# Performance work log

Hardware: AMD Instinct MI355X
Metric: run time of the kernel (lower is better)

## Reference

```python
import jax, jax.numpy as jnp
import numpy as np

EMBED_DIM = 1024
NUM_HEADS = 16
HEAD_DIM = EMBED_DIM // NUM_HEADS
B, T = 2, 2048


def setup_inputs() -> dict:
    key = jax.random.key(0)
    kx, kqkv, kout = jax.random.split(key, 3)
    x = jax.random.normal(kx, (B, T, EMBED_DIM), dtype=jnp.float32)
    # torch Linear(in, out, bias=False): y = x @ W.T, W ~ U(-1/sqrt(in), 1/sqrt(in)).
    # Store pre-transposed as (in, out) for direct matmul.
    bound = 1.0 / np.sqrt(EMBED_DIM)
    w_qkv = jax.random.uniform(kqkv, (EMBED_DIM, 3 * EMBED_DIM), dtype=jnp.float32, minval=-bound, maxval=bound)
    w_out = jax.random.uniform(kout, (EMBED_DIM, EMBED_DIM), dtype=jnp.float32, minval=-bound, maxval=bound)
    return {"x": x, "w_qkv": w_qkv, "w_out": w_out}


def reference(x, w_qkv, w_out):
    Bx, Tx, C = x.shape
    qkv = x @ w_qkv  # (B, T, 3C)
    q, k, v = jnp.split(qkv, 3, axis=-1)

    def split_heads(t):
        return t.reshape(Bx, Tx, NUM_HEADS, HEAD_DIM).transpose(0, 2, 1, 3)  # (B,H,T,hd)

    q, k, v = split_heads(q), split_heads(k), split_heads(v)
    scale = 1.0 / jnp.sqrt(jnp.float32(HEAD_DIM))
    scores = jnp.einsum("bhqd,bhkd->bhqk", q, k) * scale  # (B,H,T,T)
    causal = jnp.tril(jnp.ones((Tx, Tx), dtype=bool))  # True = keep
    scores = jnp.where(causal, scores, jnp.float32(-jnp.inf))
    weights = jax.nn.softmax(scores, axis=-1)
    out = jnp.einsum("bhqk,bhkd->bhqd", weights, v)  # (B,H,T,hd)
    out = out.transpose(0, 2, 1, 3).reshape(Bx, Tx, C)
    return out @ w_out
```

## Files before the change

kernel.cpp:

```cpp
#include <hip/hip_runtime.h>
#include <hip/hip_bf16.h>
#include <stdint.h>
#include <math.h>

#define B_ 2
#define T_ 2048
#define C_ 1024
#define H_ 16
#define HD_ 64
#define BT_ (B_*T_)
#define N1_ (3*C_)

typedef unsigned short u16;
typedef uint32_t u32;
typedef __attribute__((ext_vector_type(8))) short bf16x8;
typedef __attribute__((ext_vector_type(4))) float f32x4;
typedef __attribute__((ext_vector_type(16))) float f32x16;
typedef __attribute__((ext_vector_type(4))) unsigned int u32x4;

__device__ __forceinline__ u16 f2bf(float f) {
  __hip_bfloat16 h = __float2bfloat16(f);
  return *reinterpret_cast<u16*>(&h);
}
__device__ __forceinline__ float bf2f(u16 u) {
  u32 w = ((u32)u) << 16;
  return *reinterpret_cast<float*>(&w);
}
__device__ __forceinline__ u32 cvtpk(float lo, float hi) {
  u32 r;
  asm("v_cvt_pk_bf16_f32 %0, %1, %2" : "=v"(r) : "v"(lo), "v"(hi));
  return r;
}
__device__ __forceinline__ float exp2v(float x) {
  float r;
  asm("v_exp_f32 %0, %1" : "=v"(r) : "v"(x));
  return r;
}

__device__ __forceinline__ void gload_lds16(const void* g, void* l) {
  __builtin_amdgcn_global_load_lds(
      (const __attribute__((address_space(1))) uint32_t*)g,
      (__attribute__((address_space(3))) uint32_t*)l, 16, 0, 0);
}

#define BARX() do { asm volatile("" ::: "memory"); __builtin_amdgcn_s_barrier(); \
                    asm volatile("" ::: "memory"); } while (0)
#define LGKM0() do { asm volatile("s_waitcnt lgkmcnt(0)" ::: "memory"); \
                     __builtin_amdgcn_sched_barrier(0); } while (0)

__global__ __launch_bounds__(256) void prep_k(const float* __restrict__ x,
                                              const float* __restrict__ w_qkv,
                                              const float* __restrict__ w_out,
                                              u16* __restrict__ xb,
                                              u16* __restrict__ wqkvT,
                                              u16* __restrict__ woutT) {
  __shared__ float tile[32][33];
  int bid = blockIdx.x;
  if (bid < 4096) {
    int idx = bid * 1024 + threadIdx.x * 4;
    float4 v = *reinterpret_cast<const float4*>(x + idx);
    u16 tmp[4] = {f2bf(v.x), f2bf(v.y), f2bf(v.z), f2bf(v.w)};
    *reinterpret_cast<uint2*>(xb + idx) = *reinterpret_cast<const uint2*>(tmp);
    return;
  }
  const float* w;
  u16* wt;
  int N, tb;
  if (bid < 7168) { tb = bid - 4096; w = w_qkv; wt = wqkvT; N = N1_; }
  else            { tb = bid - 7168; w = w_out; wt = woutT; N = C_;  }
  int nx = N >> 5;
  int n0 = (tb % nx) * 32, k0 = (tb / nx) * 32;
  int tx = threadIdx.x & 31, ty = threadIdx.x >> 5;
#pragma unroll
  for (int i = 0; i < 4; i++)
    tile[ty + i*8][tx] = w[(size_t)(k0 + ty + i*8) * N + n0 + tx];
  __syncthreads();
#pragma unroll
  for (int i = 0; i < 4; i++)
    wt[(size_t)(n0 + ty + i*8) * 1024 + k0 + tx] = f2bf(tile[tx][ty + i*8]);
}

__global__ __launch_bounds__(512, 2) void gemm256(const u16* __restrict__ A, const u16* __restrict__ Bt,
                                                  u16* __restrict__ Cc) {
  __shared__ u16 As[2][256*64];
  __shared__ u16 Bs[2][192*64];
  int tid = threadIdx.x, w = tid >> 6, lane = tid & 63;
  int m0 = blockIdx.y * 256, n0 = blockIdx.x * 192;
  int wm = (w >> 2) * 128, wn = (w & 3) * 48;
  f32x4 acc[8][3] = {};

  size_t aoff[4];
  size_t boff[3];
#pragma unroll
  for (int i = 0; i < 4; i++) {
    int c = i*512 + tid, row = c >> 3;
    aoff[i] = (size_t)(m0 + row) * 1024 + (size_t)((((c & 7) ^ (row & 7))) * 8);
  }
#pragma unroll
  for (int i = 0; i < 3; i++) {
    int c = i*512 + tid, row = c >> 3;
    boff[i] = (size_t)(n0 + row) * 1024 + (size_t)((((c & 7) ^ (row & 7))) * 8);
  }
  int dstc = w * 1024;

  int r15 = lane & 15, kq = lane >> 4;
  int slot0 = (kq ^ (r15 & 7)) * 8;
  int abase = (wm + r15) * 64;
  int bbase = (wn + r15) * 64;

#pragma unroll
  for (int i = 0; i < 4; i++)
    gload_lds16(A + aoff[i], (char*)&As[0][0] + i*8192 + dstc);
#pragma unroll
  for (int i = 0; i < 3; i++)
    gload_lds16(Bt + boff[i], (char*)&Bs[0][0] + i*8192 + dstc);

  for (int t = 0; t < 16; ++t) {
    int buf = t & 1;
    const u16* Ab = &As[buf][0];
    const u16* Bb = &Bs[buf][0];
    int slot1 = slot0 ^ 32;
    bf16x8 af[8], bfv[3];

    asm volatile("s_waitcnt vmcnt(0)" ::: "memory");
    BARX();

#pragma unroll
    for (int nf = 0; nf < 3; nf++) bfv[nf] = *reinterpret_cast<const bf16x8*>(&Bb[bbase + nf*1024 + slot0]);
#pragma unroll
    for (int mf = 0; mf < 8; mf++) af[mf] = *reinterpret_cast<const bf16x8*>(&Ab[abase + mf*1024 + slot0]);
    if (t < 15) {
      int ko = (t + 1) * 64;
#pragma unroll
      for (int i = 0; i < 4; i++)
        gload_lds16(A + aoff[i] + ko, (char*)&As[buf ^ 1][0] + i*8192 + dstc);
#pragma unroll
      for (int i = 0; i < 3; i++)
        gload_lds16(Bt + boff[i] + ko, (char*)&Bs[buf ^ 1][0] + i*8192 + dstc);
    }
    BARX();
    LGKM0();
    __builtin_amdgcn_s_setprio(1);
#pragma unroll
    for (int mf = 0; mf < 8; mf++)
#pragma unroll
      for (int nf = 0; nf < 3; nf++)
        acc[mf][nf] = __builtin_amdgcn_mfma_f32_16x16x32_bf16(af[mf], bfv[nf], acc[mf][nf], 0, 0, 0);
    __builtin_amdgcn_s_setprio(0);

#pragma unroll
    for (int nf = 0; nf < 3; nf++) bfv[nf] = *reinterpret_cast<const bf16x8*>(&Bb[bbase + nf*1024 + slot1]);
#pragma unroll
    for (int mf = 0; mf < 8; mf++) af[mf] = *reinterpret_cast<const bf16x8*>(&Ab[abase + mf*1024 + slot1]);
    BARX();
    LGKM0();
    __builtin_amdgcn_s_setprio(1);
#pragma unroll
    for (int mf = 0; mf < 8; mf++)
#pragma unroll
      for (int nf = 0; nf < 3; nf++)
        acc[mf][nf] = __builtin_amdgcn_mfma_f32_16x16x32_bf16(af[mf], bfv[nf], acc[mf][nf], 0, 0, 0);
    __builtin_amdgcn_s_setprio(0);
  }

  int rg = kq * 4;
#pragma unroll
  for (int mf = 0; mf < 8; mf++)
#pragma unroll
    for (int nf = 0; nf < 3; nf++) {
      size_t basei = (size_t)(m0 + wm + mf*16 + rg) * N1_ + (size_t)(n0 + wn + nf*16 + r15);
#pragma unroll
      for (int r = 0; r < 4; r++)
        Cc[basei + (size_t)r * N1_] = f2bf(acc[mf][nf][r]);
    }
}

__global__ __launch_bounds__(512, 1) void gemm128(const u16* __restrict__ A, const u16* __restrict__ Bt,
                                                  float* __restrict__ Co) {
  __shared__ u16 As[2][128*64];
  __shared__ u16 Bs[2][128*64];
  int tid = threadIdx.x, w = tid >> 6, lane = tid & 63;
  int m0 = blockIdx.y * 128, n0 = blockIdx.x * 128;
  int wm = (w >> 2) * 64, wn = (w & 3) * 32;
  f32x4 acc[4][2] = {};

  size_t aoff[2], boff[2];
#pragma unroll
  for (int i = 0; i < 2; i++) {
    int c = i*512 + tid, row = c >> 3;
    aoff[i] = (size_t)(m0 + row) * 1024 + (size_t)((((c & 7) ^ (row & 7))) * 8);
    boff[i] = (size_t)(n0 + row) * 1024 + (size_t)((((c & 7) ^ (row & 7))) * 8);
  }
  int dstc = w * 1024;

  int r15 = lane & 15, kq = lane >> 4;
  int slot0 = (kq ^ (r15 & 7)) * 8;
  int abase = (wm + r15) * 64;
  int bbase = (wn + r15) * 64;

#pragma unroll
  for (int i = 0; i < 2; i++) {
    gload_lds16(A  + aoff[i], (char*)&As[0][0] + i*8192 + dstc);
    gload_lds16(Bt + boff[i], (char*)&Bs[0][0] + i*8192 + dstc);
  }

  for (int t = 0; t < 16; ++t) {
    int buf = t & 1;
    const u16* Ab = &As[buf][0];
    const u16* Bb = &Bs[buf][0];
    int slot1 = slot0 ^ 32;
    bf16x8 af[4], bfv[2];

    asm volatile("s_waitcnt vmcnt(0)" ::: "memory");
    BARX();

#pragma unroll
    for (int nf = 0; nf < 2; nf++) bfv[nf] = *reinterpret_cast<const bf16x8*>(&Bb[bbase + nf*1024 + slot0]);
#pragma unroll
    for (int mf = 0; mf < 4; mf++) af[mf] = *reinterpret_cast<const bf16x8*>(&Ab[abase + mf*1024 + slot0]);
    if (t < 15) {
      int ko = (t + 1) * 64;
#pragma unroll
      for (int i = 0; i < 2; i++) {
        gload_lds16(A  + aoff[i] + ko, (char*)&As[buf ^ 1][0] + i*8192 + dstc);
        gload_lds16(Bt + boff[i] + ko, (char*)&Bs[buf ^ 1][0] + i*8192 + dstc);
      }
    }
    BARX();
    LGKM0();
    __builtin_amdgcn_s_setprio(1);
#pragma unroll
    for (int mf = 0; mf < 4; mf++)
#pragma unroll
      for (int nf = 0; nf < 2; nf++)
        acc[mf][nf] = __builtin_amdgcn_mfma_f32_16x16x32_bf16(af[mf], bfv[nf], acc[mf][nf], 0, 0, 0);
    __builtin_amdgcn_s_setprio(0);

#pragma unroll
    for (int nf = 0; nf < 2; nf++) bfv[nf] = *reinterpret_cast<const bf16x8*>(&Bb[bbase + nf*1024 + slot1]);
#pragma unroll
    for (int mf = 0; mf < 4; mf++) af[mf] = *reinterpret_cast<const bf16x8*>(&Ab[abase + mf*1024 + slot1]);
    BARX();
    LGKM0();
    __builtin_amdgcn_s_setprio(1);
#pragma unroll
    for (int mf = 0; mf < 4; mf++)
#pragma unroll
      for (int nf = 0; nf < 2; nf++)
        acc[mf][nf] = __builtin_amdgcn_mfma_f32_16x16x32_bf16(af[mf], bfv[nf], acc[mf][nf], 0, 0, 0);
    __builtin_amdgcn_s_setprio(0);
  }

  int rg = kq * 4;
#pragma unroll
  for (int mf = 0; mf < 4; mf++)
#pragma unroll
    for (int nf = 0; nf < 2; nf++) {
      size_t basei = (size_t)(m0 + wm + mf*16 + rg) * C_ + (size_t)(n0 + wn + nf*16 + r15);
#pragma unroll
      for (int r = 0; r < 4; r++)
        Co[basei + (size_t)r * C_] = acc[mf][nf][r];
    }
}

__global__ __launch_bounds__(256, 2) void attn_kernel(const u16* __restrict__ qkv, u16* __restrict__ attnout) {
  __shared__ u16 Sm[4][4096];
  int tid = threadIdx.x;
  int w = tid >> 6, lane = tid & 63;
  int q31 = lane & 31, hi = lane >> 5;
  int lid = blockIdx.x;
  int xcd = lid & 7, j = lid >> 3;
  int bh = xcd * 4 + (j & 3);
  int p = j >> 2;
  int b = bh >> 4, h = bh & 15;
  const u16* base = qkv + (size_t)b * T_ * N1_;

  u16* Ks = Sm[w];
  u32* Vt32 = reinterpret_cast<u32*>(Sm[w] + 2048);

  const u16* ksrc = base + C_ + h*HD_ + (size_t)(lane >> 3) * N1_
                    + (size_t)(((lane & 7) ^ ((lane >> 3) & 7)) * 8);
  int kp2 = lane & 15, dc = (lane >> 4) * 16;
  int vcs = kp2 >> 2, vkl = kp2 & 3;
  int vflip = (lane >> 4) & 1;
  const u16* vsrc = base + 2*C_ + h*HD_ + (size_t)(2*kp2) * N1_ + dc;
  const float QSC = 0.125f * 1.44269504088896f;
  int swr = (q31 >> 1) & 3;
  int q31f = q31 ^ ((q31 >> 4) & 1);

  int sA = 63 - p, sB = p;
  int qgA = sA * 32 + q31, qgB = sB * 32 + q31;
  int nktU = sA + 1;

  bf16x8 qfA[4], qfB[4];
  {
    const u16* qrowA = base + (size_t)qgA * N1_ + h * HD_;
    const u16* qrowB = base + (size_t)qgB * N1_ + h * HD_;
#pragma unroll
    for (int kk = 0; kk < 4; kk++) {
      bf16x8 ra = *reinterpret_cast<const bf16x8*>(qrowA + kk*16 + hi*8);
      bf16x8 rb = *reinterpret_cast<const bf16x8*>(qrowB + kk*16 + hi*8);
      const u16* pa = (const u16*)&ra;
      const u16* pb = (const u16*)&rb;
      u32x4 qa, qb;
#pragma unroll
      for (int jj = 0; jj < 4; jj++) {
        qa[jj] = cvtpk(bf2f(pa[2*jj]) * QSC, bf2f(pa[2*jj+1]) * QSC);
        qb[jj] = cvtpk(bf2f(pb[2*jj]) * QSC, bf2f(pb[2*jj+1]) * QSC);
      }
      qfA[kk] = __builtin_bit_cast(bf16x8, qa);
      qfB[kk] = __builtin_bit_cast(bf16x8, qb);
    }
  }

  f32x16 oaccA[2] = {}, oaccB[2] = {};
  float lA = 0.f, lB = 0.f;

  bf16x8 vA[2], vB[2];
  {
    size_t off0 = (size_t)(w * 32) * N1_;
#pragma unroll
    for (int r = 0; r < 4; r++)
      gload_lds16(ksrc + off0 + (size_t)(8*r) * N1_, (char*)Ks + r*1024);
#pragma unroll
    for (int r = 0; r < 2; r++) {
      vA[r] = *reinterpret_cast<const bf16x8*>(vsrc + off0 + r*8);
      vB[r] = *reinterpret_cast<const bf16x8*>(vsrc + off0 + r*8 + N1_);
    }
  }

  for (int kt = w; kt < nktU; kt += 4) {
    int kb = kt * 32;
    bool lastown = (kt + 4 >= nktU);
    bool actB = (kt <= sB);

    asm volatile("s_waitcnt vmcnt(4)" ::: "memory");

    f32x16 stA = {}, stB = {};
    if (actB) {
#pragma unroll
      for (int kk = 0; kk < 4; kk++) {
        bf16x8 kf = *reinterpret_cast<const bf16x8*>(
            &Ks[q31*64 + ((((kk<<1) | hi) ^ (q31 & 7)) << 3)]);
        stA = __builtin_amdgcn_mfma_f32_32x32x16_bf16(kf, qfA[kk], stA, 0, 0, 0);
        stB = __builtin_amdgcn_mfma_f32_32x32x16_bf16(kf, qfB[kk], stB, 0, 0, 0);
      }
    } else {
#pragma unroll
      for (int kk = 0; kk < 4; kk++) {
        bf16x8 kf = *reinterpret_cast<const bf16x8*>(
            &Ks[q31*64 + ((((kk<<1) | hi) ^ (q31 & 7)) << 3)]);
        stA = __builtin_amdgcn_mfma_f32_32x32x16_bf16(kf, qfA[kk], stA, 0, 0, 0);
      }
    }
    asm volatile("s_waitcnt lgkmcnt(0)" ::: "memory");
    __builtin_amdgcn_sched_barrier(0);

    asm volatile("s_waitcnt vmcnt(0)" ::: "memory");
#pragma unroll
    for (int r2 = 0; r2 < 2; r2++) {
      const u16* au = (const u16*)&vA[r2];
      const u16* bu = (const u16*)&vB[r2];
#pragma unroll
      for (int i = 0; i < 8; i++) {
        int d = dc + r2*8 + i;
        Vt32[(d ^ vflip)*16 + ((vcs ^ ((d>>1)&3)) << 2) + vkl] = (u32)au[i] | ((u32)bu[i] << 16);
      }
    }

    if (!lastown) {
      size_t off = (size_t)(kb + 128) * N1_;
#pragma unroll
      for (int r = 0; r < 4; r++)
        gload_lds16(ksrc + off + (size_t)(8*r) * N1_, (char*)Ks + r*1024);
#pragma unroll
      for (int r = 0; r < 2; r++) {
        vA[r] = *reinterpret_cast<const bf16x8*>(vsrc + off + r*8);
        vB[r] = *reinterpret_cast<const bf16x8*>(vsrc + off + r*8 + N1_);
      }
    }

    if (kt == sA) {
#pragma unroll
      for (int r = 0; r < 16; r++) {
        int keyg = kb + (r&3) + 8*(r>>2) + 4*hi;
        if (keyg > qgA) stA[r] = -__builtin_inff();
      }
    }
    {
      float ts = 0.f;
#pragma unroll
      for (int r = 0; r < 16; r++) {
        float pp = exp2v(stA[r]);
        stA[r] = pp;
        ts += pp;
      }
      lA += ts;
    }
    bf16x8 pfA0, pfA1;
    {
      u32 pk[8];
#pragma unroll
      for (int m = 0; m < 8; m++) pk[m] = cvtpk(stA[2*m], stA[2*m+1]);
      asm volatile("v_permlane32_swap_b32 %0, %1" : "+v"(pk[0]), "+v"(pk[2]));
      asm volatile("v_permlane32_swap_b32 %0, %1" : "+v"(pk[1]), "+v"(pk[3]));
      asm volatile("v_permlane32_swap_b32 %0, %1" : "+v"(pk[4]), "+v"(pk[6]));
      asm volatile("v_permlane32_swap_b32 %0, %1" : "+v"(pk[5]), "+v"(pk[7]));
      u32x4 f0 = { pk[0], pk[1], pk[2], pk[3] };
      u32x4 f1 = { pk[4], pk[5], pk[6], pk[7] };
      pfA0 = __builtin_bit_cast(bf16x8, f0);
      pfA1 = __builtin_bit_cast(bf16x8, f1);
    }

    if (actB) {
      if (kt == sB) {
#pragma unroll
        for (int r = 0; r < 16; r++) {
          int keyg = kb + (r&3) + 8*(r>>2) + 4*hi;
          if (keyg > qgB) stB[r] = -__builtin_inff();
        }
      }
      {
        float ts = 0.f;
#pragma unroll
        for (int r = 0; r < 16; r++) {
          float pp = exp2v(stB[r]);
          stB[r] = pp;
          ts += pp;
        }
        lB += ts;
      }
      bf16x8 pfB0, pfB1;
      {
        u32 pk[8];
#pragma unroll
        for (int m = 0; m < 8; m++) pk[m] = cvtpk(stB[2*m], stB[2*m+1]);
        asm volatile("v_permlane32_swap_b32 %0, %1" : "+v"(pk[0]), "+v"(pk[2]));
        asm volatile("v_permlane32_swap_b32 %0, %1" : "+v"(pk[1]), "+v"(pk[3]));
        asm volatile("v_permlane32_swap_b32 %0, %1" : "+v"(pk[4]), "+v"(pk[6]));
        asm volatile("v_permlane32_swap_b32 %0, %1" : "+v"(pk[5]), "+v"(pk[7]));
        u32x4 f0 = { pk[0], pk[1], pk[2], pk[3] };
        u32x4 f1 = { pk[4], pk[5], pk[6], pk[7] };
        pfB0 = __builtin_bit_cast(bf16x8, f0);
        pfB1 = __builtin_bit_cast(bf16x8, f1);
      }
#pragma unroll
      for (int dt = 0; dt < 2; dt++)
#pragma unroll
        for (int kc = 0; kc < 2; kc++) {
          int cs = (kc << 1) | hi;
          bf16x8 vf = *reinterpret_cast<const bf16x8*>(
              &Vt32[(32*dt + q31f)*16 + ((cs ^ swr) << 2)]);
          oaccA[dt] = __builtin_amdgcn_mfma_f32_32x32x16_bf16(vf, kc ? pfA1 : pfA0, oaccA[dt], 0, 0, 0);
          oaccB[dt] = __builtin_amdgcn_mfma_f32_32x32x16_bf16(vf, kc ? pfB1 : pfB0, oaccB[dt], 0, 0, 0);
        }
    } else {
#pragma unroll
      for (int dt = 0; dt < 2; dt++)
#pragma unroll
        for (int kc = 0; kc < 2; kc++) {
          int cs = (kc << 1) | hi;
          bf16x8 vf = *reinterpret_cast<const bf16x8*>(
              &Vt32[(32*dt + q31f)*16 + ((cs ^ swr) << 2)]);
          oaccA[dt] = __builtin_amdgcn_mfma_f32_32x32x16_bf16(vf, kc ? pfA1 : pfA0, oaccA[dt], 0, 0, 0);
        }
    }
  }
  lA += __shfl_xor(lA, 32);
  lB += __shfl_xor(lB, 32);

  __syncthreads();
  if (w) {
    float* park = (float*)Sm[w];
#pragma unroll
    for (int dt = 0; dt < 2; dt++)
#pragma unroll
      for (int r = 0; r < 16; r++) park[(dt*16 + r)*64 + lane] = oaccA[dt][r];
    float* ml = (float*)Sm[0];
    ml[(w-1)*64 + lane] = lA;
  }
  __syncthreads();
  if (w == 0) {
    const float* ml = (const float*)Sm[0];
    float linv = 1.f / (lA + ml[lane] + ml[64 + lane] + ml[128 + lane]);
    const float* p1 = (const float*)Sm[1];
    const float* p2 = (const float*)Sm[2];
    const float* p3 = (const float*)Sm[3];
    u16* orow = attnout + (size_t)(b*T_ + qgA) * C_ + h*HD_;
#pragma unroll
    for (int dt = 0; dt < 2; dt++)
#pragma unroll
      for (int m = 0; m < 8; m++) {
        int e0 = (dt*16 + 2*m)*64 + lane, e1 = e0 + 64;
        float v0 = (oaccA[dt][2*m]   + p1[e0] + p2[e0] + p3[e0]) * linv;
        float v1 = (oaccA[dt][2*m+1] + p1[e1] + p2[e1] + p3[e1]) * linv;
        int d = 32*dt + 2*(m&1) + 8*(m>>1) + 4*hi;
        *reinterpret_cast<u32*>(orow + d) = cvtpk(v0, v1);
      }
  }
  __syncthreads();
  if (w) {
    float* park = (float*)Sm[w];
#pragma unroll
    for (int dt = 0; dt < 2; dt++)
#pragma unroll
      for (int r = 0; r < 16; r++) park[(dt*16 + r)*64 + lane] = oaccB[dt][r];
    float* ml = (float*)Sm[0];
    ml[(w-1)*64 + lane] = lB;
  }
  __syncthreads();
  if (w == 0) {
    const float* ml = (const float*)Sm[0];
    float linv = 1.f / (lB + ml[lane] + ml[64 + lane] + ml[128 + lane]);
    const float* p1 = (const float*)Sm[1];
    const float* p2 = (const float*)Sm[2];
    const float* p3 = (const float*)Sm[3];
    u16* orow = attnout + (size_t)(b*T_ + qgB) * C_ + h*HD_;
#pragma unroll
    for (int dt = 0; dt < 2; dt++)
#pragma unroll
      for (int m = 0; m < 8; m++) {
        int e0 = (dt*16 + 2*m)*64 + lane, e1 = e0 + 64;
        float v0 = (oaccB[dt][2*m]   + p1[e0] + p2[e0] + p3[e0]) * linv;
        float v1 = (oaccB[dt][2*m+1] + p1[e1] + p2[e1] + p3[e1]) * linv;
        int d = 32*dt + 2*(m&1) + 8*(m>>1) + 4*hi;
        *reinterpret_cast<u32*>(orow + d) = cvtpk(v0, v1);
      }
  }
}

extern "C" void kernel_launch(void* const* d_in, const int* in_sizes, int n_in,
                              void* d_out, int out_size, void* d_ws, size_t ws_size,
                              hipStream_t stream) {
  const float* x     = (const float*)d_in[0];
  const float* w_qkv = (const float*)d_in[1];
  const float* w_out = (const float*)d_in[2];
  float* out = (float*)d_out;
  char* ws = (char*)d_ws;
  u16* xb    = (u16*)(ws);
  u16* wqkvT = (u16*)(ws + ((size_t)8  << 20));
  u16* woutT = (u16*)(ws + ((size_t)14 << 20));
  u16* qkvb  = (u16*)(ws + ((size_t)16 << 20));
  u16* attnb = (u16*)(ws + ((size_t)40 << 20));

  prep_k<<<8192, 256, 0, stream>>>(x, w_qkv, w_out, xb, wqkvT, woutT);
  gemm256<<<dim3(16, 16), 512, 0, stream>>>(xb, wqkvT, qkvb);
  attn_kernel<<<1024, 256, 0, stream>>>(qkvb, attnb);
  gemm128<<<dim3(8, 32), 512, 0, stream>>>(attnb, woutT, out);
}
```

Before: 100.2 us.

## Load V tiles directly to LDS and gather transposed fragments at read time

V tiles are now copied straight from global memory into shared memory with direct-to-LDS loads in row-major order, as K already is. This replaces the register load, pack and transposed scatter store into LDS. Each MFMA V fragment is then assembled from eight strided 16-bit LDS reads, and the V prefetch for the next tile is issued after the PV MFMAs, with waitcnt placement adjusted to match. The aim is to drop the register staging and scatter-store work, at the cost of more, narrower LDS reads that may hit bank conflicts, and a tighter prefetch window for V.

```diff
diff --git a/kernel.cpp b/kernel.cpp
--- a/kernel.cpp
+++ b/kernel.cpp
@@ -276,17 +276,13 @@
   const u16* base = qkv + (size_t)b * T_ * N1_;
 
   u16* Ks = Sm[w];
-  u32* Vt32 = reinterpret_cast<u32*>(Sm[w] + 2048);
+  u16* Vl = Sm[w] + 2048;
 
   const u16* ksrc = base + C_ + h*HD_ + (size_t)(lane >> 3) * N1_
                     + (size_t)(((lane & 7) ^ ((lane >> 3) & 7)) * 8);
-  int kp2 = lane & 15, dc = (lane >> 4) * 16;
-  int vcs = kp2 >> 2, vkl = kp2 & 3;
-  int vflip = (lane >> 4) & 1;
-  const u16* vsrc = base + 2*C_ + h*HD_ + (size_t)(2*kp2) * N1_ + dc;
+  const u16* vsrc = base + 2*C_ + h*HD_ + (size_t)(lane >> 3) * N1_
+                    + (size_t)((lane & 7) * 8);
   const float QSC = 0.125f * 1.44269504088896f;
-  int swr = (q31 >> 1) & 3;
-  int q31f = q31 ^ ((q31 >> 4) & 1);
 
   int sA = 63 - p, sB = p;
   int qgA = sA * 32 + q31, qgB = sB * 32 + q31;
@@ -316,17 +312,14 @@
   f32x16 oaccA[2] = {}, oaccB[2] = {};
   float lA = 0.f, lB = 0.f;
 
-  bf16x8 vA[2], vB[2];
   {
     size_t off0 = (size_t)(w * 32) * N1_;
 #pragma unroll
     for (int r = 0; r < 4; r++)
       gload_lds16(ksrc + off0 + (size_t)(8*r) * N1_, (char*)Ks + r*1024);
 #pragma unroll
-    for (int r = 0; r < 2; r++) {
-      vA[r] = *reinterpret_cast<const bf16x8*>(vsrc + off0 + r*8);
-      vB[r] = *reinterpret_cast<const bf16x8*>(vsrc + off0 + r*8 + N1_);
-    }
+    for (int r = 0; r < 4; r++)
+      gload_lds16(vsrc + off0 + (size_t)(8*r) * N1_, (char*)Vl + r*1024);
   }
 
   for (int kt = w; kt < nktU; kt += 4) {
@@ -356,28 +349,11 @@
     asm volatile("s_waitcnt lgkmcnt(0)" ::: "memory");
     __builtin_amdgcn_sched_barrier(0);
 
-    asm volatile("s_waitcnt vmcnt(0)" ::: "memory");
-#pragma unroll
-    for (int r2 = 0; r2 < 2; r2++) {
-      const u16* au = (const u16*)&vA[r2];
-      const u16* bu = (const u16*)&vB[r2];
-#pragma unroll
-      for (int i = 0; i < 8; i++) {
-        int d = dc + r2*8 + i;
-        Vt32[(d ^ vflip)*16 + ((vcs ^ ((d>>1)&3)) << 2) + vkl] = (u32)au[i] | ((u32)bu[i] << 16);
-      }
-    }
-
     if (!lastown) {
       size_t off = (size_t)(kb + 128) * N1_;
 #pragma unroll
       for (int r = 0; r < 4; r++)
         gload_lds16(ksrc + off + (size_t)(8*r) * N1_, (char*)Ks + r*1024);
-#pragma unroll
-      for (int r = 0; r < 2; r++) {
-        vA[r] = *reinterpret_cast<const bf16x8*>(vsrc + off + r*8);
-        vB[r] = *reinterpret_cast<const bf16x8*>(vsrc + off + r*8 + N1_);
-      }
     }
 
     if (kt == sA) {
@@ -411,7 +387,7 @@
       pfA0 = __builtin_bit_cast(bf16x8, f0);
       pfA1 = __builtin_bit_cast(bf16x8, f1);
     }
-
+    bf16x8 pfB0, pfB1;
     if (actB) {
       if (kt == sB) {
 #pragma unroll
@@ -430,40 +406,55 @@
         }
         lB += ts;
       }
-      bf16x8 pfB0, pfB1;
-      {
-        u32 pk[8];
-#pragma unroll
-        for (int m = 0; m < 8; m++) pk[m] = cvtpk(stB[2*m], stB[2*m+1]);
-        asm volatile("v_permlane32_swap_b32 %0, %1" : "+v"(pk[0]), "+v"(pk[2]));
-        asm volatile("v_permlane32_swap_b32 %0, %1" : "+v"(pk[1]), "+v"(pk[3]));
-        asm volatile("v_permlane32_swap_b32 %0, %1" : "+v"(pk[4]), "+v"(pk[6]));
-        asm volatile("v_permlane32_swap_b32 %0, %1" : "+v"(pk[5]), "+v"(pk[7]));
-        u32x4 f0 = { pk[0], pk[1], pk[2], pk[3] };
-        u32x4 f1 = { pk[4], pk[5], pk[6], pk[7] };
-        pfB0 = __builtin_bit_cast(bf16x8, f0);
-        pfB1 = __builtin_bit_cast(bf16x8, f1);
-      }
+      u32 pk[8];
+#pragma unroll
+      for (int m = 0; m < 8; m++) pk[m] = cvtpk(stB[2*m], stB[2*m+1]);
+      asm volatile("v_permlane32_swap_b32 %0, %1" : "+v"(pk[0]), "+v"(pk[2]));
+      asm volatile("v_permlane32_swap_b32 %0, %1" : "+v"(pk[1]), "+v"(pk[3]));
+      asm volatile("v_permlane32_swap_b32 %0, %1" : "+v"(pk[4]), "+v"(pk[6]));
+      asm volatile("v_permlane32_swap_b32 %0, %1" : "+v"(pk[5]), "+v"(pk[7]));
+      u32x4 f0 = { pk[0], pk[1], pk[2], pk[3] };
+      u32x4 f1 = { pk[4], pk[5], pk[6], pk[7] };
+      pfB0 = __builtin_bit_cast(bf16x8, f0);
+      pfB1 = __builtin_bit_cast(bf16x8, f1);
+    }
+
+    if (!lastown) asm volatile("s_waitcnt vmcnt(4)" ::: "memory");
+    else          asm volatile("s_waitcnt vmcnt(0)" ::: "memory");
+
+    if (actB) {
 #pragma unroll
       for (int dt = 0; dt < 2; dt++)
 #pragma unroll
-        for (int kc = 0; kc < 2; kc++) {
-          int cs = (kc << 1) | hi;
-          bf16x8 vf = *reinterpret_cast<const bf16x8*>(
-              &Vt32[(32*dt + q31f)*16 + ((cs ^ swr) << 2)]);
-          oaccA[dt] = __builtin_amdgcn_mfma_f32_32x32x16_bf16(vf, kc ? pfA1 : pfA0, oaccA[dt], 0, 0, 0);
-          oaccB[dt] = __builtin_amdgcn_mfma_f32_32x32x16_bf16(vf, kc ? pfB1 : pfB0, oaccB[dt], 0, 0, 0);
+        for (int ks = 0; ks < 2; ks++) {
+          u16 tv[8];
+#pragma unroll
+          for (int jj = 0; jj < 8; jj++)
+            tv[jj] = Vl[(16*ks + 8*hi + jj)*64 + 32*dt + q31];
+          bf16x8 vf = *reinterpret_cast<const bf16x8*>(tv);
+          oaccA[dt] = __builtin_amdgcn_mfma_f32_32x32x16_bf16(vf, ks ? pfA1 : pfA0, oaccA[dt], 0, 0, 0);
+          oaccB[dt] = __builtin_amdgcn_mfma_f32_32x32x16_bf16(vf, ks ? pfB1 : pfB0, oaccB[dt], 0, 0, 0);
         }
     } else {
 #pragma unroll
       for (int dt = 0; dt < 2; dt++)
 #pragma unroll
-        for (int kc = 0; kc < 2; kc++) {
-          int cs = (kc << 1) | hi;
-          bf16x8 vf = *reinterpret_cast<const bf16x8*>(
-              &Vt32[(32*dt + q31f)*16 + ((cs ^ swr) << 2)]);
-          oaccA[dt] = __builtin_amdgcn_mfma_f32_32x32x16_bf16(vf, kc ? pfA1 : pfA0, oaccA[dt], 0, 0, 0);
+        for (int ks = 0; ks < 2; ks++) {
+          u16 tv[8];
+#pragma unroll
+          for (int jj = 0; jj < 8; jj++)
+            tv[jj] = Vl[(16*ks + 8*hi + jj)*64 + 32*dt + q31];
+          bf16x8 vf = *reinterpret_cast<const bf16x8*>(tv);
+          oaccA[dt] = __builtin_amdgcn_mfma_f32_32x32x16_bf16(vf, ks ? pfA1 : pfA0, oaccA[dt], 0, 0, 0);
         }
+    }
+    LGKM0();
+
+    if (!lastown) {
+      size_t off = (size_t)(kb + 128) * N1_;
+#pragma unroll
+      for (int r = 0; r < 4; r++)
+        gload_lds16(vsrc + off + (size_t)(8*r) * N1_, (char*)Vl + r*1024);
     }
   }
   lA += __shfl_xor(lA, 32);
```

Measured after the change: 96.39 us. -3.8%, faster.
